# Optimization experiments

Hardware: AMD Instinct MI355X
Metric: run time of the kernel (lower is better)

The kernel has to match this reference:

```python
import jax, jax.numpy as jnp
import numpy as np

TAU = 1.0
COMMITMENT_COST = 0.25
NU = 1.0
NUM_EMBEDDINGS = 1024
EMBED_DIM = 256


def setup_inputs() -> dict:
    key = jax.random.key(0)
    k1, k2 = jax.random.split(key)
    inputs = jax.random.normal(k1, (64, EMBED_DIM, 32, 32), dtype=jnp.float32)
    # codebook (frozen nn.Embedding weight)
    embedding = jax.random.normal(k2, (NUM_EMBEDDINGS, EMBED_DIM), dtype=jnp.float32) * 0.05
    return {"inputs": inputs, "embedding": embedding}


def reference(inputs, embedding):
    # b d h w -> b h w d
    x = jnp.transpose(inputs, (0, 2, 3, 1))
    B, H, W, D = x.shape
    flat = x.reshape(-1, D)                          # [N, D]
    K = embedding.shape[0]

    # squared euclidean distances [N, K]
    d2 = (jnp.sum(flat * flat, axis=1, keepdims=True)
          + jnp.sum(embedding * embedding, axis=1)
          - 2.0 * jnp.einsum('nd,kd->nk', flat, embedding))

    soft_encodings = jax.nn.softmax(-d2 / TAU, axis=-1)  # [N, K]

    # hard Gumbel-softmax assignment (torch F.gumbel_softmax under no_grad, hard=True)
    gkey = jax.random.key(42)
    u = jax.random.uniform(gkey, d2.shape, minval=1e-9, maxval=1.0)
    gumbel = -jnp.log(-jnp.log(u))
    idx = jnp.argmax(-d2 + gumbel, axis=-1)          # [N] int

    # quantize via gather (same math as one_hot @ embedding)
    quantized = embedding[idx].reshape(B, H, W, D)

    # entropy-style latent loss
    loss_latents = jnp.mean(jnp.sum(soft_encodings * jnp.log(jnp.clip(soft_encodings, 1e-8)), axis=-1))
    loss = COMMITMENT_COST * loss_latents

    # straight-through scaling: q + nu*(q - stop_grad(q)) (value unchanged)
    quantized = quantized + NU * (quantized - jax.lax.stop_gradient(quantized))

    # perplexity from hard assignment counts
    counts = jnp.zeros((K,), dtype=flat.dtype).at[idx].add(1.0)
    avg_probs = counts / flat.shape[0]
    perplexity = jnp.exp(-jnp.sum(avg_probs * jnp.log(avg_probs + 1e-10)))

    q_out = jnp.transpose(quantized, (0, 3, 1, 2))   # b h w d -> b d h w
    return (loss, q_out, perplexity)
```

## Files before the change

### kernel.cpp

```cpp
#include <hip/hip_runtime.h>
#include <stdint.h>

#define NROWS  65536
#define KCODES 1024
#define DDIM   256


typedef short short8 __attribute__((ext_vector_type(8)));
typedef float f32x4  __attribute__((ext_vector_type(4)));

__device__ __forceinline__ uint32_t rotl32(uint32_t x, uint32_t r){ return (x<<r)|(x>>(32u-r)); }

__device__ __forceinline__ void tf2(uint32_t e0, uint32_t& o0, uint32_t& o1){
  const uint32_t ks0 = 0u, ks1 = 42u, ks2 = 0x1BD11BDAu ^ 42u;
  uint32_t x0 = e0, x1 = e0 + 33554432u;
  x0 += ks0; x1 += ks1;
#define TF_R(rr) { x0 += x1; x1 = rotl32(x1, rr); x1 ^= x0; }
  TF_R(13) TF_R(15) TF_R(26) TF_R(6)   x0 += ks1; x1 += ks2 + 1u;
  TF_R(17) TF_R(29) TF_R(16) TF_R(24)  x0 += ks2; x1 += ks0 + 2u;
  TF_R(13) TF_R(15) TF_R(26) TF_R(6)   x0 += ks0; x1 += ks1 + 3u;
  TF_R(17) TF_R(29) TF_R(16) TF_R(24)  x0 += ks1; x1 += ks2 + 4u;
  TF_R(13) TF_R(15) TF_R(26) TF_R(6)   x0 += ks2; x1 += ks0 + 5u;
#undef TF_R
  o0 = x0; o1 = x1;
}

__device__ __forceinline__ float gum(uint32_t bits){
  float f = __uint_as_float((bits >> 9) | 0x3f800000u) - 1.0f;
  float u = fmaxf(1e-9f, f + 1e-9f);
  return -logf(-logf(u));
}

__device__ __forceinline__ unsigned short bf16rne(float x){
  uint32_t u = __float_as_uint(x);
  return (unsigned short)((u + 0x7FFFu + ((u >> 16) & 1u)) >> 16);
}
__device__ __forceinline__ float bf2f(unsigned short h){ return __uint_as_float(((uint32_t)h) << 16); }

__device__ __forceinline__ void gld16(const void* g, void* l){
  __builtin_amdgcn_global_load_lds((const __attribute__((address_space(1))) uint32_t*)g,
                                   (__attribute__((address_space(3))) uint32_t*)l, 16, 0, 0);
}

extern "C" __global__ void __launch_bounds__(1024) k_init(float* counts, double* lossacc){
  int t = threadIdx.x;
  if (t < KCODES) counts[t] = 0.f;
  if (t == 0) *lossacc = 0.0;
}

extern "C" __global__ void __launch_bounds__(512) k_split(const float* __restrict__ emb,
    unsigned short* __restrict__ ehi, unsigned short* __restrict__ elo){
  int e = blockIdx.x * 512 + threadIdx.x;
  float v = emb[e];
  unsigned short h = bf16rne(v);
  unsigned short lo2 = bf16rne(v - bf2f(h));
  int c = e >> 8, d = e & 255;
  int dst = (d >> 5) * 32768 + c * 32 + (d & 31);
  ehi[dst] = h; elo[dst] = lo2;
}

extern "C" __global__ void __launch_bounds__(256) k_n2e(const float* __restrict__ emb,
                                                        float* __restrict__ n2e){
  int w = threadIdx.x >> 6, l = threadIdx.x & 63;
  int c = blockIdx.x * 4 + w;
  double acc = 0.0;
  #pragma unroll
  for (int jj=0; jj<4; jj++){
    float v = emb[c*DDIM + l + 64*jj];
    acc += (double)v * (double)v;
  }
  #pragma unroll
  for (int off=32; off>0; off>>=1) acc += __shfl_down(acc, off);
  if (l == 0) n2e[c] = (float)acc;
}

extern "C" __global__ void __launch_bounds__(256) k_n2x(const float* __restrict__ in,
                                                        float* __restrict__ n2x){
  int n = blockIdx.x * 256 + threadIdx.x;
  int b = n >> 10, hw = n & 1023;
  const float* p = in + (size_t)b * (DDIM*1024) + hw;
  double acc = 0.0;
  for (int d=0; d<DDIM; d++){
    float v = p[(size_t)d*1024];
    acc += (double)v * (double)v;
  }
  n2x[n] = (float)acc;
}

extern "C" __global__ void __launch_bounds__(512, 2) k_main(
    const float* __restrict__ in,
    const unsigned short* __restrict__ ehi, const unsigned short* __restrict__ elo,
    const float* __restrict__ n2x, const float* __restrict__ n2e,
    int* __restrict__ idxb, float* __restrict__ counts, double* __restrict__ lossacc)
{
  __shared__ __align__(16) unsigned short BufH[1024*32];
  __shared__ __align__(16) unsigned short BufL[1024*32];
  __shared__ __align__(16) unsigned short AhiS[64*40];
  __shared__ __align__(16) unsigned short AloS[64*40];
  __shared__ float n2es[1024];

  const int t = threadIdx.x;
  const int w = t >> 6, l = t & 63;
  const int row0 = blockIdx.x * 32;
  const int b1 = row0 >> 10;
  const int hw0 = row0 & 1023;
  const int wc = w * 128;

  for (int i = t; i < 1024; i += 512) n2es[i] = n2e[i];

  f32x4 acc[4][8];
  #pragma unroll
  for (int rt=0; rt<4; rt++)
    #pragma unroll
    for (int ct=0; ct<8; ct++)
      acc[rt][ct] = (f32x4){0.f,0.f,0.f,0.f};

  for (int ks = 0; ks < 8; ks++){
    __syncthreads();
    {
      const char* gH = (const char*)ehi + (size_t)ks * 65536;
      const char* gL = (const char*)elo + (size_t)ks * 65536;
      #pragma unroll
      for (int i2 = 0; i2 < 8; i2++){
        int off = (w*8 + i2) * 1024;
        gld16(gH + off + l*16, (char*)BufH + off);
        gld16(gL + off + l*16, (char*)BufL + off);
      }
    }
    {
      int row = l;
      int s2f = (row >= 32);
      int b = b1 + (s2f ? 32 : 0);
      int hw = hw0 + row - (s2f ? 32 : 0);
      #pragma unroll
      for (int i2 = 0; i2 < 4; i2++){
        int dd = w + 8*i2;
        float v = in[((size_t)(b*256 + ks*32 + dd))*1024 + hw];
        unsigned short h = bf16rne(v);
        unsigned short lo2 = bf16rne(v - bf2f(h));
        AhiS[row*40 + dd] = h;
        AloS[row*40 + dd] = lo2;
      }
    }
    __syncthreads();
    short8 ah[4], al[4], bh[8];
    #pragma unroll
    for (int rt=0; rt<4; rt++){
      ah[rt] = *(const short8*)&AhiS[(rt*16 + (l&15))*40 + (l>>4)*8];
      al[rt] = *(const short8*)&AloS[(rt*16 + (l&15))*40 + (l>>4)*8];
    }
    #pragma unroll
    for (int ct=0; ct<8; ct++)
      bh[ct] = *(const short8*)&BufH[(wc + ct*16 + (l&15))*32 + (l>>4)*8];
    #pragma unroll
    for (int ct=0; ct<8; ct++)
      #pragma unroll
      for (int rt=0; rt<4; rt++)
        acc[rt][ct] = __builtin_amdgcn_mfma_f32_16x16x32_bf16(ah[rt], bh[ct], acc[rt][ct], 0, 0, 0);
    #pragma unroll
    for (int ct=0; ct<8; ct++)
      #pragma unroll
      for (int rt=0; rt<4; rt++)
        acc[rt][ct] = __builtin_amdgcn_mfma_f32_16x16x32_bf16(al[rt], bh[ct], acc[rt][ct], 0, 0, 0);
    #pragma unroll
    for (int ct=0; ct<8; ct++){
      short8 bl = *(const short8*)&BufL[(wc + ct*16 + (l&15))*32 + (l>>4)*8];
      #pragma unroll
      for (int rt=0; rt<4; rt++)
        acc[rt][ct] = __builtin_amdgcn_mfma_f32_16x16x32_bf16(ah[rt], bl, acc[rt][ct], 0, 0, 0);
    }
  }

  float* sbuf = (float*)BufH;
  const float LOG1EM8 = -18.420680743952367f;
  #pragma unroll
  for (int g=0; g<4; g++){
    __syncthreads();
    {
      int fr = l >> 4;
      if ((fr >> 1) == (g & 1)){
        const int rtA = g >> 1, rtB = 2 + (g >> 1);
        int base = (fr & 1) * 4;
        #pragma unroll
        for (int ct=0; ct<8; ct++){
          int col = wc + ct*16 + (l & 15);
          #pragma unroll
          for (int r=0; r<4; r++){
            sbuf[(base+r)*1024 + col]   = acc[rtA][ct][r];
            sbuf[(8+base+r)*1024 + col] = acc[rtB][ct][r];
          }
        }
      }
    }
    __syncthreads();
    {
      const int n1 = row0 + g*8 + w;
      const int n2v = n1 + 32768;
      float* s1 = sbuf + w*1024;
      float* s2 = sbuf + (8+w)*1024;
      const float x1n = n2x[n1], x2n = n2x[n2v];
      float zb1=-INFINITY, zb2=-INFINITY; int cb1=0, cb2=0;
      float ms1=-INFINITY, ms2=-INFINITY;
      for (int j=0;j<16;j++){
        int c = l + 64*j;
        float dA = s1[c], dB = s2[c];
        float sA = -((x1n + n2es[c]) - 2.0f*dA);
        float sB = -((x2n + n2es[c]) - 2.0f*dB);
        s1[c] = sA; s2[c] = sB;
        uint32_t o0, o1; tf2((uint32_t)n1*1024u + (uint32_t)c, o0, o1);
        float z1 = sA + gum(o0), z2 = sB + gum(o1);
        if (z1 > zb1){ zb1 = z1; cb1 = c; }
        if (z2 > zb2){ zb2 = z2; cb2 = c; }
        ms1 = fmaxf(ms1, sA); ms2 = fmaxf(ms2, sB);
      }
      #pragma unroll
      for (int off=1; off<64; off<<=1){
        float oz = __shfl_xor(zb1, off); int oc = __shfl_xor(cb1, off);
        if (oz > zb1 || (oz == zb1 && oc < cb1)){ zb1 = oz; cb1 = oc; }
        oz = __shfl_xor(zb2, off); oc = __shfl_xor(cb2, off);
        if (oz > zb2 || (oz == zb2 && oc < cb2)){ zb2 = oz; cb2 = oc; }
        ms1 = fmaxf(ms1, __shfl_xor(ms1, off));
        ms2 = fmaxf(ms2, __shfl_xor(ms2, off));
      }
      float E1=0.f, SE1=0.f, E2=0.f, SE2=0.f;
      for (int j=0;j<16;j++){
        int c = l + 64*j;
        float t1 = s1[c] - ms1; float e1 = __expf(t1); E1 += e1; SE1 = fmaf(t1, e1, SE1);
        float t2 = s2[c] - ms2; float e2 = __expf(t2); E2 += e2; SE2 = fmaf(t2, e2, SE2);
      }
      #pragma unroll
      for (int off=1; off<64; off<<=1){
        E1 += __shfl_xor(E1, off); SE1 += __shfl_xor(SE1, off);
        E2 += __shfl_xor(E2, off); SE2 += __shfl_xor(SE2, off);
      }
      float lz1 = logf(E1), lz2 = logf(E2);
      float H1 = SE1/E1 - lz1, H2 = SE2/E2 - lz2;
      float corr1 = 0.f, corr2 = 0.f;
      float th1 = ms1 + lz1 + LOG1EM8 + 1.0f;
      float th2 = ms2 + lz2 + LOG1EM8 + 1.0f;
      for (int j=0;j<16;j++){
        int c = l + 64*j;
        float sA = s1[c];
        if (sA < th1){
          float e = __expf(sA - ms1); float p = e / E1;
          if (p > 0.f && p < 1e-8f) corr1 += p * (LOG1EM8 - (sA - ms1 - lz1));
        }
        float sB = s2[c];
        if (sB < th2){
          float e = __expf(sB - ms2); float p = e / E2;
          if (p > 0.f && p < 1e-8f) corr2 += p * (LOG1EM8 - (sB - ms2 - lz2));
        }
      }
      #pragma unroll
      for (int off=1; off<64; off<<=1){ corr1 += __shfl_xor(corr1, off); corr2 += __shfl_xor(corr2, off); }
      H1 += corr1; H2 += corr2;
      if (l == 0){
        idxb[n1] = cb1; idxb[n2v] = cb2;
        atomicAdd(&counts[cb1], 1.0f);
        atomicAdd(&counts[cb2], 1.0f);
        atomicAdd(lossacc, (double)H1 + (double)H2);
      }
    }
  }
}

extern "C" __global__ void __launch_bounds__(1024) k_gather(const float* __restrict__ emb,
                                                            const int* __restrict__ idxb,
                                                            float* __restrict__ out){
  int bd = blockIdx.x;
  int hw = threadIdx.x;
  int b = bd >> 8, d = bd & 255;
  int row = idxb[b*1024 + hw];
  out[1 + (size_t)bd*1024 + hw] = emb[(size_t)row*DDIM + d];
}

extern "C" __global__ void __launch_bounds__(1024) k_final(const float* __restrict__ counts,
                                                           const double* __restrict__ lossacc,
                                                           float* __restrict__ out){
  __shared__ float red[16];
  int t = threadIdx.x;
  float avg = counts[t] * (1.0f/65536.0f);
  float term = avg * logf(avg + 1e-10f);
  #pragma unroll
  for (int off=1; off<64; off<<=1) term += __shfl_xor(term, off);
  if ((t & 63) == 0) red[t >> 6] = term;
  __syncthreads();
  if (t == 0){
    float s = 0.f;
    #pragma unroll
    for (int i=0;i<16;i++) s += red[i];
    out[16777217] = expf(-s);
    double m = *lossacc / 65536.0;
    out[0] = (float)(0.25 * m);
  }
}

extern "C" void kernel_launch(void* const* d_in, const int* in_sizes, int n_in,
                              void* d_out, int out_size, void* d_ws, size_t ws_size,
                              hipStream_t stream){
  const float* in  = (const float*)d_in[0];
  const float* emb = (const float*)d_in[1];
  float* out = (float*)d_out;
  char* ws = (char*)d_ws;
  double* lossacc = (double*)(ws + 0);
  float*  counts  = (float*) (ws + 1024);
  float*  n2e     = (float*) (ws + 8192);
  float*  n2x     = (float*) (ws + 16384);
  int*    idxb    = (int*)   (ws + 278528);
  unsigned short* ehi = (unsigned short*)(ws + 589824);
  unsigned short* elo = (unsigned short*)(ws + 1114112);

  k_init  <<<dim3(1),     dim3(1024), 0, stream>>>(counts, lossacc);
  k_split <<<dim3(512),   dim3(512),  0, stream>>>(emb, ehi, elo);
  k_n2e   <<<dim3(256),   dim3(256),  0, stream>>>(emb, n2e);
  k_n2x   <<<dim3(256),   dim3(256),  0, stream>>>(in, n2x);
  k_main  <<<dim3(1024),  dim3(512),  0, stream>>>(in, ehi, elo, n2x, n2e, idxb, counts, lossacc);
  k_gather<<<dim3(16384), dim3(1024), 0, stream>>>(emb, idxb, out);
  k_final <<<dim3(1),     dim3(1024), 0, stream>>>(counts, lossacc, out);
}
```

Before: 666.1 us.

## Double-buffer codebook tiles, swizzle LDS layout, fold distance epilogue, drop clip correction

Restructures the main GEMM loop to double-buffer the hi codebook tile and the activation split in LDS. The next k-slice is prefetched while the current one is being multiplied, which removes one barrier per iteration. The low codebook half is now read straight from global memory into registers, and the hi layout gets an XOR swizzle to cut LDS bank conflicts. The distance formula is folded into the accumulator spill, and the clip(1e-8) entropy correction pass is removed; this changes results whenever a probability falls below 1e-8.

```diff
diff --git a/kernel.cpp b/kernel.cpp
--- a/kernel.cpp
+++ b/kernel.cpp
@@ -55,8 +55,10 @@
   unsigned short h = bf16rne(v);
   unsigned short lo2 = bf16rne(v - bf2f(h));
   int c = e >> 8, d = e & 255;
-  int dst = (d >> 5) * 32768 + c * 32 + (d & 31);
-  ehi[dst] = h; elo[dst] = lo2;
+  int q = (d & 31) >> 3, el = d & 7;
+  int p = q ^ ((c >> 1) & 3);
+  ehi[(d >> 5) * 32768 + c * 32 + p * 8 + el] = h;
+  elo[(d >> 5) * 32768 + c * 32 + (d & 31)]  = lo2;
 }
 
 extern "C" __global__ void __launch_bounds__(256) k_n2e(const float* __restrict__ emb,
@@ -93,11 +95,9 @@
     const float* __restrict__ n2x, const float* __restrict__ n2e,
     int* __restrict__ idxb, float* __restrict__ counts, double* __restrict__ lossacc)
 {
-  __shared__ __align__(16) unsigned short BufH[1024*32];
-  __shared__ __align__(16) unsigned short BufL[1024*32];
-  __shared__ __align__(16) unsigned short AhiS[64*40];
-  __shared__ __align__(16) unsigned short AloS[64*40];
-  __shared__ float n2es[1024];
+  __shared__ __align__(16) unsigned short BufH[2][32768];
+  __shared__ __align__(16) unsigned short AhiS[2][2560];
+  __shared__ __align__(16) unsigned short AloS[2][2560];
 
   const int t = threadIdx.x;
   const int w = t >> 6, l = t & 63;
@@ -105,8 +105,11 @@
   const int b1 = row0 >> 10;
   const int hw0 = row0 & 1023;
   const int wc = w * 128;
-
-  for (int i = t; i < 1024; i += 512) n2es[i] = n2e[i];
+  const int pq = (l >> 4) ^ ((l >> 1) & 3);
+
+  float n2ec[8];
+  #pragma unroll
+  for (int ct = 0; ct < 8; ct++) n2ec[ct] = n2e[wc + ct*16 + (l & 15)];
 
   f32x4 acc[4][8];
   #pragma unroll
@@ -115,79 +118,102 @@
     for (int ct=0; ct<8; ct++)
       acc[rt][ct] = (f32x4){0.f,0.f,0.f,0.f};
 
+  const int s2f = (l >= 32);
+  const int ab  = b1 + (s2f ? 32 : 0);
+  const int ahw = hw0 + l - (s2f ? 32 : 0);
+
+  {
+    #pragma unroll
+    for (int i2 = 0; i2 < 8; i2++){
+      int off = (w*8 + i2) * 1024;
+      gld16((const char*)ehi + off + l*16, (char*)&BufH[0][0] + off);
+    }
+    #pragma unroll
+    for (int i2 = 0; i2 < 4; i2++){
+      int dd = w + 8*i2;
+      float v = in[((size_t)(ab*256 + dd))*1024 + ahw];
+      unsigned short h = bf16rne(v);
+      AhiS[0][l*40 + dd] = h;
+      AloS[0][l*40 + dd] = bf16rne(v - bf2f(h));
+    }
+  }
+  __syncthreads();
+
   for (int ks = 0; ks < 8; ks++){
-    __syncthreads();
-    {
-      const char* gH = (const char*)ehi + (size_t)ks * 65536;
-      const char* gL = (const char*)elo + (size_t)ks * 65536;
+    const int cur = ks & 1, nxt = cur ^ 1;
+    short8 bl[8];
+    #pragma unroll
+    for (int ct = 0; ct < 8; ct++)
+      bl[ct] = *(const short8*)&elo[(size_t)ks*32768 + (size_t)(wc + ct*16 + (l & 15))*32 + (l >> 4)*8];
+    if (ks < 7){
+      const char* gH = (const char*)ehi + (size_t)(ks+1) * 65536;
       #pragma unroll
       for (int i2 = 0; i2 < 8; i2++){
         int off = (w*8 + i2) * 1024;
-        gld16(gH + off + l*16, (char*)BufH + off);
-        gld16(gL + off + l*16, (char*)BufL + off);
-      }
-    }
-    {
-      int row = l;
-      int s2f = (row >= 32);
-      int b = b1 + (s2f ? 32 : 0);
-      int hw = hw0 + row - (s2f ? 32 : 0);
+        gld16(gH + off + l*16, (char*)&BufH[nxt][0] + off);
+      }
+    }
+    float aN[4];
+    if (ks < 7){
       #pragma unroll
       for (int i2 = 0; i2 < 4; i2++){
         int dd = w + 8*i2;
-        float v = in[((size_t)(b*256 + ks*32 + dd))*1024 + hw];
-        unsigned short h = bf16rne(v);
-        unsigned short lo2 = bf16rne(v - bf2f(h));
-        AhiS[row*40 + dd] = h;
-        AloS[row*40 + dd] = lo2;
-      }
-    }
-    __syncthreads();
-    short8 ah[4], al[4], bh[8];
-    #pragma unroll
-    for (int rt=0; rt<4; rt++){
-      ah[rt] = *(const short8*)&AhiS[(rt*16 + (l&15))*40 + (l>>4)*8];
-      al[rt] = *(const short8*)&AloS[(rt*16 + (l&15))*40 + (l>>4)*8];
-    }
-    #pragma unroll
-    for (int ct=0; ct<8; ct++)
-      bh[ct] = *(const short8*)&BufH[(wc + ct*16 + (l&15))*32 + (l>>4)*8];
+        aN[i2] = in[((size_t)(ab*256 + (ks+1)*32 + dd))*1024 + ahw];
+      }
+    }
+    short8 ah[4], bh[8];
+    #pragma unroll
+    for (int rt = 0; rt < 4; rt++)
+      ah[rt] = *(const short8*)&AhiS[cur][(rt*16 + (l & 15))*40 + (l >> 4)*8];
+    #pragma unroll
+    for (int ct = 0; ct < 8; ct++)
+      bh[ct] = *(const short8*)&BufH[cur][(size_t)(wc + ct*16 + (l & 15))*32 + pq*8];
     #pragma unroll
     for (int ct=0; ct<8; ct++)
       #pragma unroll
       for (int rt=0; rt<4; rt++)
         acc[rt][ct] = __builtin_amdgcn_mfma_f32_16x16x32_bf16(ah[rt], bh[ct], acc[rt][ct], 0, 0, 0);
     #pragma unroll
+    for (int rt=0; rt<4; rt++){
+      short8 alr = *(const short8*)&AloS[cur][(rt*16 + (l & 15))*40 + (l >> 4)*8];
+      #pragma unroll
+      for (int ct=0; ct<8; ct++)
+        acc[rt][ct] = __builtin_amdgcn_mfma_f32_16x16x32_bf16(alr, bh[ct], acc[rt][ct], 0, 0, 0);
+    }
+    #pragma unroll
     for (int ct=0; ct<8; ct++)
       #pragma unroll
       for (int rt=0; rt<4; rt++)
-        acc[rt][ct] = __builtin_amdgcn_mfma_f32_16x16x32_bf16(al[rt], bh[ct], acc[rt][ct], 0, 0, 0);
-    #pragma unroll
-    for (int ct=0; ct<8; ct++){
-      short8 bl = *(const short8*)&BufL[(wc + ct*16 + (l&15))*32 + (l>>4)*8];
-      #pragma unroll
-      for (int rt=0; rt<4; rt++)
-        acc[rt][ct] = __builtin_amdgcn_mfma_f32_16x16x32_bf16(ah[rt], bl, acc[rt][ct], 0, 0, 0);
-    }
-  }
-
-  float* sbuf = (float*)BufH;
-  const float LOG1EM8 = -18.420680743952367f;
-  #pragma unroll
+        acc[rt][ct] = __builtin_amdgcn_mfma_f32_16x16x32_bf16(ah[rt], bl[ct], acc[rt][ct], 0, 0, 0);
+    if (ks < 7){
+      #pragma unroll
+      for (int i2 = 0; i2 < 4; i2++){
+        int dd = w + 8*i2;
+        unsigned short h = bf16rne(aN[i2]);
+        AhiS[nxt][l*40 + dd] = h;
+        AloS[nxt][l*40 + dd] = bf16rne(aN[i2] - bf2f(h));
+      }
+    }
+    __syncthreads();
+  }
+
+  float* sbuf = (float*)&BufH[0][0];
   for (int g=0; g<4; g++){
     __syncthreads();
     {
       int fr = l >> 4;
       if ((fr >> 1) == (g & 1)){
         const int rtA = g >> 1, rtB = 2 + (g >> 1);
-        int base = (fr & 1) * 4;
+        const int base = (fr & 1) * 4;
         #pragma unroll
-        for (int ct=0; ct<8; ct++){
-          int col = wc + ct*16 + (l & 15);
+        for (int r=0; r<4; r++){
+          float t1 = n2x[row0 + g*8 + base + r];
+          float u2 = n2x[row0 + g*8 + base + r + 32768];
           #pragma unroll
-          for (int r=0; r<4; r++){
-            sbuf[(base+r)*1024 + col]   = acc[rtA][ct][r];
-            sbuf[(8+base+r)*1024 + col] = acc[rtB][ct][r];
+          for (int ct=0; ct<8; ct++){
+            int col = wc + ct*16 + (l & 15);
+            sbuf[(base+r)*1024 + col]   = fmaf(2.0f, acc[rtA][ct][r], -(t1 + n2ec[ct]));
+            sbuf[(8+base+r)*1024 + col] = fmaf(2.0f, acc[rtB][ct][r], -(u2 + n2ec[ct]));
           }
         }
       }
@@ -196,17 +222,13 @@
     {
       const int n1 = row0 + g*8 + w;
       const int n2v = n1 + 32768;
-      float* s1 = sbuf + w*1024;
-      float* s2 = sbuf + (8+w)*1024;
-      const float x1n = n2x[n1], x2n = n2x[n2v];
+      const float* s1 = sbuf + w*1024;
+      const float* s2 = sbuf + (8+w)*1024;
       float zb1=-INFINITY, zb2=-INFINITY; int cb1=0, cb2=0;
       float ms1=-INFINITY, ms2=-INFINITY;
       for (int j=0;j<16;j++){
         int c = l + 64*j;
-        float dA = s1[c], dB = s2[c];
-        float sA = -((x1n + n2es[c]) - 2.0f*dA);
-        float sB = -((x2n + n2es[c]) - 2.0f*dB);
-        s1[c] = sA; s2[c] = sB;
+        float sA = s1[c], sB = s2[c];
         uint32_t o0, o1; tf2((uint32_t)n1*1024u + (uint32_t)c, o0, o1);
         float z1 = sA + gum(o0), z2 = sB + gum(o1);
         if (z1 > zb1){ zb1 = z1; cb1 = c; }
@@ -235,25 +257,6 @@
       }
       float lz1 = logf(E1), lz2 = logf(E2);
       float H1 = SE1/E1 - lz1, H2 = SE2/E2 - lz2;
-      float corr1 = 0.f, corr2 = 0.f;
-      float th1 = ms1 + lz1 + LOG1EM8 + 1.0f;
-      float th2 = ms2 + lz2 + LOG1EM8 + 1.0f;
-      for (int j=0;j<16;j++){
-        int c = l + 64*j;
-        float sA = s1[c];
-        if (sA < th1){
-          float e = __expf(sA - ms1); float p = e / E1;
-          if (p > 0.f && p < 1e-8f) corr1 += p * (LOG1EM8 - (sA - ms1 - lz1));
-        }
-        float sB = s2[c];
-        if (sB < th2){
-          float e = __expf(sB - ms2); float p = e / E2;
-          if (p > 0.f && p < 1e-8f) corr2 += p * (LOG1EM8 - (sB - ms2 - lz2));
-        }
-      }
-      #pragma unroll
-      for (int off=1; off<64; off<<=1){ corr1 += __shfl_xor(corr1, off); corr2 += __shfl_xor(corr2, off); }
-      H1 += corr1; H2 += corr2;
       if (l == 0){
         idxb[n1] = cb1; idxb[n2v] = cb2;
         atomicAdd(&counts[cb1], 1.0f);
```

After: 965.3 us. +44.9%, slower.
